# Optimization experiments

Hardware: AMD Instinct MI355X
Metric: run time of the kernel (lower is better)

## Reference

```python
import jax, jax.numpy as jnp
import numpy as np

EPS = 1e-12
ALPHA = 0.5


def mlp(x, W1, b1, W2, b2):
    # 2-layer MLP (dropout inactive in eval mode) + row-wise l2 norm * 10
    h = jax.nn.relu(x @ W1 + b1)
    y = h @ W2 + b2
    n = jnp.maximum(jnp.linalg.norm(y, axis=-1, keepdims=True), EPS)
    return y / n * 10.0


def setup_inputs() -> dict:
    key = jax.random.key(0)
    ks = jax.random.split(key, 12)
    T, N, F = 3, 100000, 128
    M, E = 4, 65536
    B, H, O = 65536, 128, 64
    X = jax.random.normal(ks[0], (T, N, F), dtype=jnp.float32)
    s_features = jax.random.normal(ks[1], (B, F), dtype=jnp.float32)
    features_map = jax.random.randint(ks[2], (T, N), 0, N)
    s_idxs = jax.random.randint(ks[3], (M, T, E), 0, B)
    t_idxs = jax.random.randint(ks[4], (M, T, E), 0, N)
    weightss = jax.random.uniform(ks[5], (M, T, E), dtype=jnp.float32)
    W1 = jax.random.normal(ks[6], (F, H), dtype=jnp.float32) / np.sqrt(F)
    b1 = jnp.zeros((H,), dtype=jnp.float32)
    W2 = jax.random.normal(ks[7], (H, O), dtype=jnp.float32) / np.sqrt(H)
    b2 = jnp.zeros((O,), dtype=jnp.float32)
    metapath_weights = jnp.ones((M,), dtype=jnp.float32)
    ntype_weights = jnp.ones((T,), dtype=jnp.float32)
    return {"X": X, "s_features": s_features, "features_map": features_map,
            "s_idxs": s_idxs, "t_idxs": t_idxs, "weightss": weightss,
            "batch_size": B, "W1": W1, "b1": b1, "W2": W2, "b2": b2,
            "metapath_weights": metapath_weights, "ntype_weights": ntype_weights}


def reference(X, s_features, features_map, s_idxs, t_idxs, weightss,
              batch_size, W1, b1, W2, b2, metapath_weights, ntype_weights):
    M, T, E = s_idxs.shape
    O = W2.shape[1]
    nm = jax.nn.softmax(metapath_weights)  # [M]
    nt = jax.nn.softmax(ntype_weights)     # [T]
    t_arr = jnp.arange(T)[None, :, None]   # [1,T,1]
    map_idx = features_map[t_arr, t_idxs]  # [M,T,E]
    feats = X[t_arr, map_idx]              # [M,T,E,F] gather
    y = mlp(feats, W1, b1, W2, b2)         # [M,T,E,O]
    # fold metapath & type weights into per-edge weights (scatter is linear)
    ew = weightss * nt[None, :, None] * nm[:, None, None]  # [M,T,E]
    contrib = (y * ew[..., None]).reshape(-1, O)
    seg = s_idxs.reshape(-1)
    out = jax.ops.segment_sum(contrib, seg, num_segments=batch_size)  # [B,O]
    out = (1.0 - ALPHA) * out + ALPHA * mlp(s_features, W1, b1, W2, b2)
    return jax.nn.log_softmax(out, axis=1)
```

## Files before the change

### kernel.cpp

```cpp
#include <hip/hip_runtime.h>

#define Fdim 128
#define Hdim 128
#define Odim 64
#define RT 64
#define ECAP 64
#define NMLP 448
#define NSCAT 64
#define EPSV 1e-12f
#define ALPHAV 0.5f

typedef _Float16 h8_t __attribute__((ext_vector_type(8)));
typedef _Float16 h4_t __attribute__((ext_vector_type(4)));
typedef float f32x4 __attribute__((ext_vector_type(4)));

#define W2T_OFF 0
#define X_OFF   16384
#define H_OFF   32768
#define LDS_BYTES 49152
#define WIMG_BYTES 49152

extern "C" __global__ __launch_bounds__(512, 4)
void fused_mlp_scatter(const float* __restrict__ X, const float* __restrict__ S,
                       const char* __restrict__ wimg, const float* __restrict__ b1,
                       const float* __restrict__ b2,
                       _Float16* __restrict__ Yh, float* __restrict__ out,
                       int TN, int rows_total, int ngroups,
                       const int* __restrict__ s_idxs, const int* __restrict__ t_idxs,
                       const float* __restrict__ wss, const int* __restrict__ fmap,
                       const float* __restrict__ mw, const float* __restrict__ tw,
                       int* __restrict__ cnt, int2* __restrict__ edat,
                       int Nn, int Tt, int Mm, int Eslab)
{
    const int tid = threadIdx.x;

    if (blockIdx.x >= NMLP) {
        if (edat == nullptr) return;
        const int sb = blockIdx.x - NMLP;
        float mmax = -1e30f, tmax = -1e30f, msum = 0.f, tsum = 0.f;
        for (int i = 0; i < Mm; ++i) mmax = fmaxf(mmax, mw[i]);
        for (int i = 0; i < Mm; ++i) msum += expf(mw[i] - mmax);
        for (int i = 0; i < Tt; ++i) tmax = fmaxf(tmax, tw[i]);
        for (int i = 0; i < Tt; ++i) tsum += expf(tw[i] - tmax);
        const float inv = (1.0f - ALPHAV) / (msum * tsum);

        const int MT = Mm * Tt;
        for (int slab = 0; slab < MT; ++slab) {
            const int t  = slab % Tt;
            const int tN = t * Nn;
            const float scale = expf(mw[slab / Tt] - mmax) * expf(tw[t] - tmax) * inv;
            for (int i = sb * 512 + tid; i < Eslab; i += NSCAT * 512) {
                int e    = slab * Eslab + i;
                int si   = s_idxs[e];
                int yrow = tN + fmap[tN + t_idxs[e]];
                float w  = wss[e] * scale;
                int pos  = atomicAdd(cnt + si, 1);
                if (pos < ECAP)
                    edat[(size_t)si * ECAP + pos] = make_int2(yrow, __float_as_int(w));
            }
        }
        return;
    }

    extern __shared__ char smem[];
    const int wave = tid >> 6;
    const int lane = tid & 63;
    const int c = lane & 15;
    const int g = lane >> 4;

    #pragma unroll
    for (int i = 0; i < 2; ++i) {
        int idx = tid + i * 512;
        float4 v = *(const float4*)(wimg + 32768 + idx * 16);
        *(float4*)(smem + W2T_OFF + idx * 16) = v;
    }

    h8_t w1f[4];
    {
        int r0 = wave * 16 + c;
        #pragma unroll
        for (int kt = 0; kt < 4; ++kt)
            w1f[kt] = *(const h8_t*)(wimg + (((r0 << 8) + (kt << 6) + (g << 4)) ^ ((c & 7) << 4)));
    }

    const int hbase = wave * 16 + 4 * g;
    float b1v[4];
    #pragma unroll
    for (int j = 0; j < 4; ++j) b1v[j] = b1[hbase + j];
    float bb[4];
    #pragma unroll
    for (int ct = 0; ct < 4; ++ct) bb[ct] = b2[ct * 16 + c];

    float4 pf[4];
    int grp = blockIdx.x;
    #pragma unroll
    for (int it = 0; it < 4; ++it) {
        int idx = tid + it * 512;
        int r = idx >> 5, c4 = idx & 31;
        int rowg = grp * RT + r;
        float4 v = make_float4(0.f, 0.f, 0.f, 0.f);
        if (rowg < TN)               v = *(const float4*)(X + (size_t)rowg * Fdim + c4 * 4);
        else if (rowg < rows_total)  v = *(const float4*)(S + (size_t)(rowg - TN) * Fdim + c4 * 4);
        pf[it] = v;
    }
    #pragma unroll
    for (int it = 0; it < 4; ++it) {
        int idx = tid + it * 512;
        int r = idx >> 5, c4 = idx & 31;
        h4_t hv;
        hv[0] = (_Float16)pf[it].x; hv[1] = (_Float16)pf[it].y;
        hv[2] = (_Float16)pf[it].z; hv[3] = (_Float16)pf[it].w;
        *(h4_t*)(smem + X_OFF + ((r * 256 + c4 * 8) ^ ((r & 7) << 4))) = hv;
    }
    __syncthreads();

    for (; grp < ngroups; grp += NMLP) {
        const int gnext = grp + NMLP;

        #pragma unroll
        for (int it = 0; it < 4; ++it) {
            int idx = tid + it * 512;
            int r = idx >> 5, c4 = idx & 31;
            int rowg = gnext * RT + r;
            float4 v = make_float4(0.f, 0.f, 0.f, 0.f);
            if (rowg < TN)               v = *(const float4*)(X + (size_t)rowg * Fdim + c4 * 4);
            else if (rowg < rows_total)  v = *(const float4*)(S + (size_t)(rowg - TN) * Fdim + c4 * 4);
            pf[it] = v;
        }

        f32x4 acc[4];
        #pragma unroll
        for (int r = 0; r < 4; ++r) acc[r] = (f32x4){0.f, 0.f, 0.f, 0.f};

        #pragma unroll
        for (int kt = 0; kt < 4; ++kt) {
            #pragma unroll
            for (int rt = 0; rt < 4; ++rt) {
                int xr = rt * 16 + c;
                h8_t bf = *(const h8_t*)(smem + X_OFF + ((xr * 256 + kt * 64 + g * 16) ^ ((c & 7) << 4)));
                acc[rt] = __builtin_amdgcn_mfma_f32_16x16x32_f16(w1f[kt], bf, acc[rt], 0, 0, 0);
            }
        }

        #pragma unroll
        for (int rt = 0; rt < 4; ++rt) {
            int xr = rt * 16 + c;
            h4_t hv;
            #pragma unroll
            for (int j = 0; j < 4; ++j) {
                float hval = acc[rt][j] + b1v[j];
                hval = fmaxf(hval, 0.f);
                hv[j] = (_Float16)hval;
            }
            *(h4_t*)(smem + H_OFF + ((xr * 256 + hbase * 2) ^ ((xr & 7) << 4))) = hv;
        }
        __syncthreads();

        if (wave < 4) {
            f32x4 acc2[4];
            #pragma unroll
            for (int ct = 0; ct < 4; ++ct) acc2[ct] = (f32x4){0.f, 0.f, 0.f, 0.f};

            #pragma unroll
            for (int kt = 0; kt < 4; ++kt) {
                int xr = wave * 16 + c;
                h8_t a = *(const h8_t*)(smem + H_OFF + ((xr * 256 + kt * 64 + g * 16) ^ ((xr & 7) << 4)));
                #pragma unroll
                for (int ct = 0; ct < 4; ++ct) {
                    int wr = ct * 16 + c;
                    h8_t bf = *(const h8_t*)(smem + W2T_OFF + ((wr * 256 + kt * 64 + g * 16) ^ ((c & 7) << 4)));
                    acc2[ct] = __builtin_amdgcn_mfma_f32_16x16x32_f16(a, bf, acc2[ct], 0, 0, 0);
                }
            }

            float y[4][4];
            float ssq[4] = {0.f, 0.f, 0.f, 0.f};
            #pragma unroll
            for (int ct = 0; ct < 4; ++ct) {
                #pragma unroll
                for (int j = 0; j < 4; ++j) {
                    float v = acc2[ct][j] + bb[ct];
                    y[ct][j] = v;
                    ssq[j] += v * v;
                }
            }
            #pragma unroll
            for (int j = 0; j < 4; ++j) {
                float s = ssq[j];
                s += __shfl_xor(s, 1);
                s += __shfl_xor(s, 2);
                s += __shfl_xor(s, 4);
                s += __shfl_xor(s, 8);
                float n  = fmaxf(sqrtf(s), EPSV);
                float sc = 10.0f / n;
                int rowg = grp * RT + wave * 16 + 4 * g + j;
                if (rowg < TN) {
                    _Float16* dst = Yh + (size_t)rowg * Odim;
                    #pragma unroll
                    for (int ct = 0; ct < 4; ++ct)
                        dst[ct * 16 + c] = (_Float16)(y[ct][j] * sc);
                } else if (rowg < rows_total) {
                    float* dst = out + (size_t)(rowg - TN) * Odim;
                    #pragma unroll
                    for (int ct = 0; ct < 4; ++ct)
                        dst[ct * 16 + c] = ALPHAV * y[ct][j] * sc;
                }
            }
        }

        #pragma unroll
        for (int it = 0; it < 4; ++it) {
            int idx = tid + it * 512;
            int r = idx >> 5, c4 = idx & 31;
            h4_t hv;
            hv[0] = (_Float16)pf[it].x; hv[1] = (_Float16)pf[it].y;
            hv[2] = (_Float16)pf[it].z; hv[3] = (_Float16)pf[it].w;
            *(h4_t*)(smem + X_OFF + ((r * 256 + c4 * 8) ^ ((r & 7) << 4))) = hv;
        }
        __syncthreads();
    }
}

extern "C" __global__ __launch_bounds__(256)
void prep_all(const float* __restrict__ W1, const float* __restrict__ W2,
              char* __restrict__ wimg, int* __restrict__ cnt, int B)
{
    if (blockIdx.x < 96) {
        int idx = blockIdx.x * 256 + threadIdx.x;
        if (idx < 16384) {
            int h = idx >> 7, f = idx & 127;
            float v = W1[(size_t)f * Hdim + h];
            int byte = (h * 256 + f * 2) ^ ((h & 7) << 4);
            *(_Float16*)(wimg + byte) = (_Float16)v;
        } else if (idx < 24576) {
            int i2 = idx - 16384;
            int o = i2 >> 7, k = i2 & 127;
            float v = W2[(size_t)k * Odim + o];
            int byte = 32768 + ((o * 256 + k * 2) ^ ((o & 7) << 4));
            *(_Float16*)(wimg + byte) = (_Float16)v;
        }
    } else {
        int i = (blockIdx.x - 96) * 256 + threadIdx.x;
        if (i < B) cnt[i] = 0;
    }
}

extern "C" __global__ __launch_bounds__(256)
void row_gather(const int2* __restrict__ edgedat, const int* __restrict__ cnt,
                const _Float16* __restrict__ Yh, float* __restrict__ out, int B)
{
    const int lane = threadIdx.x & 63;
    const int grp8 = lane >> 3;
    const int sub  = lane & 7;
    int b = blockIdx.x * 4 + (threadIdx.x >> 6);
    if (b >= B) return;
    int n = cnt[b];
    if (n > ECAP) n = ECAP;
    const int2* ebase = edgedat + (size_t)b * ECAP;

    float acc[8];
    #pragma unroll
    for (int j = 0; j < 8; ++j) acc[j] = 0.f;

    for (int e = grp8; e < n; e += 8) {
        int2 ed = ebase[e];
        float w = __int_as_float(ed.y);
        h8_t y8 = *(const h8_t*)(Yh + (size_t)ed.x * Odim + sub * 8);
        #pragma unroll
        for (int j = 0; j < 8; ++j) acc[j] += w * (float)y8[j];
    }
    #pragma unroll
    for (int d = 8; d < 64; d <<= 1) {
        #pragma unroll
        for (int j = 0; j < 8; ++j) acc[j] += __shfl_xor(acc[j], d);
    }
    const float* orow = out + (size_t)b * Odim + sub * 8;
    float v[8];
    #pragma unroll
    for (int j = 0; j < 8; ++j) v[j] = orow[j] + acc[j];

    float mx = v[0];
    #pragma unroll
    for (int j = 1; j < 8; ++j) mx = fmaxf(mx, v[j]);
    #pragma unroll
    for (int d = 1; d < 8; d <<= 1) mx = fmaxf(mx, __shfl_xor(mx, d));
    float sm = 0.f;
    #pragma unroll
    for (int j = 0; j < 8; ++j) sm += expf(v[j] - mx);
    #pragma unroll
    for (int d = 1; d < 8; d <<= 1) sm += __shfl_xor(sm, d);
    float lg = mx + logf(sm);

    if (grp8 == 0) {
        float* dst = out + (size_t)b * Odim + sub * 8;
        #pragma unroll
        for (int j = 0; j < 8; ++j) dst[j] = v[j] - lg;
    }
}


extern "C" __global__ __launch_bounds__(256)
void edge_scatter(const int* __restrict__ s_idxs, const int* __restrict__ t_idxs,
                  const float* __restrict__ weightss, const int* __restrict__ fmap,
                  const _Float16* __restrict__ Yh, const float* __restrict__ mw,
                  const float* __restrict__ tw,
                  float* __restrict__ out, int Nn, int Tt, int Mm, int Eslab)
{
    const int lane = threadIdx.x & 63;
    const int slab = blockIdx.y;
    const int t    = slab % Tt;
    const int tN   = t * Nn;
    float mmax = -1e30f, tmax = -1e30f, msum = 0.f, tsum = 0.f;
    for (int i = 0; i < Mm; ++i) mmax = fmaxf(mmax, mw[i]);
    for (int i = 0; i < Mm; ++i) msum += expf(mw[i] - mmax);
    for (int i = 0; i < Tt; ++i) tmax = fmaxf(tmax, tw[i]);
    for (int i = 0; i < Tt; ++i) tsum += expf(tw[i] - tmax);
    const float scale = (1.0f - ALPHAV) * expf(mw[slab / Tt] - mmax) * expf(tw[t] - tmax)
                        / (msum * tsum);

    const int wid  = blockIdx.x * (blockDim.x >> 6) + (threadIdx.x >> 6);
    const int off  = wid * 64;
    if (off >= Eslab) return;

    const int ebase = slab * Eslab + off;
    int   e_ok = (off + lane) < Eslab;
    int   eidx = ebase + (e_ok ? lane : 0);
    int   si   = s_idxs[eidx];
    int   ti   = t_idxs[eidx];
    float w    = e_ok ? (weightss[eidx] * scale) : 0.0f;
    int   yrow = tN + fmap[tN + ti];

    #pragma unroll 8
    for (int i = 0; i < 64; ++i) {
        int   nd = __builtin_amdgcn_readlane(yrow, i);
        int   s  = __builtin_amdgcn_readlane(si, i);
        float ws = __uint_as_float(__builtin_amdgcn_readlane(__float_as_uint(w), i));
        float yv = (float)Yh[(size_t)nd * Odim + lane];
        atomicAdd(out + (size_t)s * Odim + lane, yv * ws);
    }
}

extern "C" __global__ __launch_bounds__(256)
void log_softmax_rows(float* __restrict__ out, int Brows)
{
    int lane = threadIdx.x & 63;
    int r = blockIdx.x * 4 + (threadIdx.x >> 6);
    if (r >= Brows) return;
    float* row = out + (size_t)r * Odim;
    float v = row[lane];
    float mx = v;
    for (int off = 32; off > 0; off >>= 1) mx = fmaxf(mx, __shfl_xor(mx, off));
    float ex = expf(v - mx);
    float s = ex;
    for (int off = 32; off > 0; off >>= 1) s += __shfl_xor(s, off);
    row[lane] = v - mx - logf(s);
}

extern "C" void kernel_launch(void* const* d_in, const int* in_sizes, int n_in,
                              void* d_out, int out_size, void* d_ws, size_t ws_size,
                              hipStream_t stream)
{
    const float* X   = (const float*)d_in[0];
    const float* S   = (const float*)d_in[1];
    const int*   fmap= (const int*)d_in[2];
    const int*   sidx= (const int*)d_in[3];
    const int*   tidx= (const int*)d_in[4];
    const float* wss = (const float*)d_in[5];
    const float* W1  = (const float*)d_in[7];
    const float* b1  = (const float*)d_in[8];
    const float* W2  = (const float*)d_in[9];
    const float* b2  = (const float*)d_in[10];
    const float* mw  = (const float*)d_in[11];
    const float* tw  = (const float*)d_in[12];
    float* out = (float*)d_out;

    const int M = in_sizes[11];
    const int T = in_sizes[12];
    const int H = in_sizes[8];
    const int Fv = in_sizes[7] / H;
    const int N = in_sizes[2] / T;
    const int nedges = in_sizes[3];
    const int E = nedges / (M * T);
    const int B = in_sizes[1] / Fv;
    const int TN = T * N;
    const int rows_total = TN + B;
    const int ngroups = (rows_total + RT - 1) / RT;

    char* wp = (char*)d_ws;
    size_t used = 0;
    auto alloc = [&](size_t bytes) -> char* {
        char* p = wp + used;
        used = (used + bytes + 255) & ~(size_t)255;
        return p;
    };
    _Float16* Yh   = (_Float16*)alloc((size_t)TN * Odim * sizeof(_Float16));
    char*     wimg = (char*)    alloc((size_t)WIMG_BYTES);
    int*      cntp = (int*)     alloc((size_t)B * sizeof(int));
    int2*     edat = (int2*)    alloc((size_t)B * ECAP * sizeof(int2));
    bool bucket_ok = used <= ws_size;

    hipFuncSetAttribute((const void*)fused_mlp_scatter,
                        hipFuncAttributeMaxDynamicSharedMemorySize, LDS_BYTES);

    const int zb = (B + 255) / 256;
    prep_all<<<96 + zb, 256, 0, stream>>>(W1, W2, wimg, cntp, B);

    if (bucket_ok) {
        fused_mlp_scatter<<<NMLP + NSCAT, 512, LDS_BYTES, stream>>>(
            X, S, wimg, b1, b2, Yh, out, TN, rows_total, ngroups,
            sidx, tidx, wss, fmap, mw, tw, cntp, edat, N, T, M, E);
        row_gather<<<(B + 3) / 4, 256, 0, stream>>>(edat, cntp, Yh, out, B);
    } else {
        fused_mlp_scatter<<<NMLP + NSCAT, 512, LDS_BYTES, stream>>>(
            X, S, wimg, b1, b2, Yh, out, TN, rows_total, ngroups,
            sidx, tidx, wss, fmap, mw, tw, cntp, nullptr, N, T, M, E);
        int waves_per_slab = (E + 63) / 64;
        dim3 sg((waves_per_slab + 3) / 4, M * T);
        edge_scatter<<<sg, 256, 0, stream>>>(sidx, tidx, wss, fmap, Yh, mw, tw, out,
                                             N, T, M, E);
        log_softmax_rows<<<(B + 3) / 4, 256, 0, stream>>>(out, B);
    }
}
```

Baseline: 147.6 us.

## Split edge bucketing into its own kernel and double-buffer MLP LDS tiles

Moves edge bucketing out of the fused MLP kernel into a separate fully parallel scatter_edges kernel (one thread per edge, one grid row per slab) that runs before the MLP. The MLP kernel now uses double-buffered X and H tiles in LDS, so the next tile is written before the barrier and one __syncthreads per iteration is dropped. Its grid becomes 512 blocks with a gridDim stride. LDS grows from 48KB to 80KB, which may cut occupancy, and the bucketing no longer overlaps with MLP work.

```diff
diff --git a/kernel.cpp b/kernel.cpp
--- a/kernel.cpp
+++ b/kernel.cpp
@@ -5,8 +5,6 @@
 #define Odim 64
 #define RT 64
 #define ECAP 64
-#define NMLP 448
-#define NSCAT 64
 #define EPSV 1e-12f
 #define ALPHAV 0.5f
 
@@ -15,54 +13,20 @@
 typedef float f32x4 __attribute__((ext_vector_type(4)));
 
 #define W2T_OFF 0
-#define X_OFF   16384
-#define H_OFF   32768
-#define LDS_BYTES 49152
+#define X0_OFF  16384
+#define H0_OFF  49152
+#define LDS_BYTES 81920
 #define WIMG_BYTES 49152
 
 extern "C" __global__ __launch_bounds__(512, 4)
-void fused_mlp_scatter(const float* __restrict__ X, const float* __restrict__ S,
-                       const char* __restrict__ wimg, const float* __restrict__ b1,
-                       const float* __restrict__ b2,
-                       _Float16* __restrict__ Yh, float* __restrict__ out,
-                       int TN, int rows_total, int ngroups,
-                       const int* __restrict__ s_idxs, const int* __restrict__ t_idxs,
-                       const float* __restrict__ wss, const int* __restrict__ fmap,
-                       const float* __restrict__ mw, const float* __restrict__ tw,
-                       int* __restrict__ cnt, int2* __restrict__ edat,
-                       int Nn, int Tt, int Mm, int Eslab)
-{
-    const int tid = threadIdx.x;
-
-    if (blockIdx.x >= NMLP) {
-        if (edat == nullptr) return;
-        const int sb = blockIdx.x - NMLP;
-        float mmax = -1e30f, tmax = -1e30f, msum = 0.f, tsum = 0.f;
-        for (int i = 0; i < Mm; ++i) mmax = fmaxf(mmax, mw[i]);
-        for (int i = 0; i < Mm; ++i) msum += expf(mw[i] - mmax);
-        for (int i = 0; i < Tt; ++i) tmax = fmaxf(tmax, tw[i]);
-        for (int i = 0; i < Tt; ++i) tsum += expf(tw[i] - tmax);
-        const float inv = (1.0f - ALPHAV) / (msum * tsum);
-
-        const int MT = Mm * Tt;
-        for (int slab = 0; slab < MT; ++slab) {
-            const int t  = slab % Tt;
-            const int tN = t * Nn;
-            const float scale = expf(mw[slab / Tt] - mmax) * expf(tw[t] - tmax) * inv;
-            for (int i = sb * 512 + tid; i < Eslab; i += NSCAT * 512) {
-                int e    = slab * Eslab + i;
-                int si   = s_idxs[e];
-                int yrow = tN + fmap[tN + t_idxs[e]];
-                float w  = wss[e] * scale;
-                int pos  = atomicAdd(cnt + si, 1);
-                if (pos < ECAP)
-                    edat[(size_t)si * ECAP + pos] = make_int2(yrow, __float_as_int(w));
-            }
-        }
-        return;
-    }
-
+void mlp_all(const float* __restrict__ X, const float* __restrict__ S,
+             const char* __restrict__ wimg, const float* __restrict__ b1,
+             const float* __restrict__ b2,
+             _Float16* __restrict__ Yh, float* __restrict__ out,
+             int TN, int rows_total, int ngroups)
+{
     extern __shared__ char smem[];
+    const int tid  = threadIdx.x;
     const int wave = tid >> 6;
     const int lane = tid & 63;
     const int c = lane & 15;
@@ -110,12 +74,16 @@
         h4_t hv;
         hv[0] = (_Float16)pf[it].x; hv[1] = (_Float16)pf[it].y;
         hv[2] = (_Float16)pf[it].z; hv[3] = (_Float16)pf[it].w;
-        *(h4_t*)(smem + X_OFF + ((r * 256 + c4 * 8) ^ ((r & 7) << 4))) = hv;
+        *(h4_t*)(smem + X0_OFF + ((r * 256 + c4 * 8) ^ ((r & 7) << 4))) = hv;
     }
     __syncthreads();
 
-    for (; grp < ngroups; grp += NMLP) {
-        const int gnext = grp + NMLP;
+    int cur = 0;
+    for (; grp < ngroups; grp += gridDim.x, cur ^= 1) {
+        const int gnext = grp + gridDim.x;
+        const int xb = X0_OFF + cur * 16384;
+        const int hb = H0_OFF + cur * 16384;
+        const int xn = X0_OFF + (cur ^ 1) * 16384;
 
         #pragma unroll
         for (int it = 0; it < 4; ++it) {
@@ -137,7 +105,7 @@
             #pragma unroll
             for (int rt = 0; rt < 4; ++rt) {
                 int xr = rt * 16 + c;
-                h8_t bf = *(const h8_t*)(smem + X_OFF + ((xr * 256 + kt * 64 + g * 16) ^ ((c & 7) << 4)));
+                h8_t bf = *(const h8_t*)(smem + xb + ((xr * 256 + kt * 64 + g * 16) ^ ((c & 7) << 4)));
                 acc[rt] = __builtin_amdgcn_mfma_f32_16x16x32_f16(w1f[kt], bf, acc[rt], 0, 0, 0);
             }
         }
@@ -152,8 +120,19 @@
                 hval = fmaxf(hval, 0.f);
                 hv[j] = (_Float16)hval;
             }
-            *(h4_t*)(smem + H_OFF + ((xr * 256 + hbase * 2) ^ ((xr & 7) << 4))) = hv;
-        }
+            *(h4_t*)(smem + hb + ((xr * 256 + hbase * 2) ^ ((xr & 7) << 4))) = hv;
+        }
+
+        #pragma unroll
+        for (int it = 0; it < 4; ++it) {
+            int idx = tid + it * 512;
+            int r = idx >> 5, c4 = idx & 31;
+            h4_t hv;
+            hv[0] = (_Float16)pf[it].x; hv[1] = (_Float16)pf[it].y;
+            hv[2] = (_Float16)pf[it].z; hv[3] = (_Float16)pf[it].w;
+            *(h4_t*)(smem + xn + ((r * 256 + c4 * 8) ^ ((r & 7) << 4))) = hv;
+        }
+
         __syncthreads();
 
         if (wave < 4) {
@@ -164,7 +143,7 @@
             #pragma unroll
             for (int kt = 0; kt < 4; ++kt) {
                 int xr = wave * 16 + c;
-                h8_t a = *(const h8_t*)(smem + H_OFF + ((xr * 256 + kt * 64 + g * 16) ^ ((xr & 7) << 4)));
+                h8_t a = *(const h8_t*)(smem + hb + ((xr * 256 + kt * 64 + g * 16) ^ ((xr & 7) << 4)));
                 #pragma unroll
                 for (int ct = 0; ct < 4; ++ct) {
                     int wr = ct * 16 + c;
@@ -207,17 +186,6 @@
                 }
             }
         }
-
-        #pragma unroll
-        for (int it = 0; it < 4; ++it) {
-            int idx = tid + it * 512;
-            int r = idx >> 5, c4 = idx & 31;
-            h4_t hv;
-            hv[0] = (_Float16)pf[it].x; hv[1] = (_Float16)pf[it].y;
-            hv[2] = (_Float16)pf[it].z; hv[3] = (_Float16)pf[it].w;
-            *(h4_t*)(smem + X_OFF + ((r * 256 + c4 * 8) ^ ((r & 7) << 4))) = hv;
-        }
-        __syncthreads();
     }
 }
 
@@ -246,6 +214,35 @@
 }
 
 extern "C" __global__ __launch_bounds__(256)
+void scatter_edges(const int* __restrict__ s_idxs, const int* __restrict__ t_idxs,
+                   const float* __restrict__ wss, const int* __restrict__ fmap,
+                   const float* __restrict__ mw, const float* __restrict__ tw,
+                   int* __restrict__ cnt, int2* __restrict__ edat,
+                   int Nn, int Tt, int Mm, int Eslab)
+{
+    const int slab = blockIdx.y;
+    const int t    = slab % Tt;
+    const int tN   = t * Nn;
+    float mmax = -1e30f, tmax = -1e30f, msum = 0.f, tsum = 0.f;
+    for (int i = 0; i < Mm; ++i) mmax = fmaxf(mmax, mw[i]);
+    for (int i = 0; i < Mm; ++i) msum += expf(mw[i] - mmax);
+    for (int i = 0; i < Tt; ++i) tmax = fmaxf(tmax, tw[i]);
+    for (int i = 0; i < Tt; ++i) tsum += expf(tw[i] - tmax);
+    const float scale = (1.0f - ALPHAV) * expf(mw[slab / Tt] - mmax) * expf(tw[t] - tmax)
+                        / (msum * tsum);
+
+    int i = blockIdx.x * 256 + threadIdx.x;
+    if (i >= Eslab) return;
+    int e = slab * Eslab + i;
+    int si   = s_idxs[e];
+    int yrow = tN + fmap[tN + t_idxs[e]];
+    float w  = wss[e] * scale;
+    int pos = atomicAdd(cnt + si, 1);
+    if (pos < ECAP)
+        edat[(size_t)si * ECAP + pos] = make_int2(yrow, __float_as_int(w));
+}
+
+extern "C" __global__ __launch_bounds__(256)
 void row_gather(const int2* __restrict__ edgedat, const int* __restrict__ cnt,
                 const _Float16* __restrict__ Yh, float* __restrict__ out, int B)
 {
@@ -399,21 +396,22 @@
     int2*     edat = (int2*)    alloc((size_t)B * ECAP * sizeof(int2));
     bool bucket_ok = used <= ws_size;
 
-    hipFuncSetAttribute((const void*)fused_mlp_scatter,
+    hipFuncSetAttribute((const void*)mlp_all,
                         hipFuncAttributeMaxDynamicSharedMemorySize, LDS_BYTES);
 
     const int zb = (B + 255) / 256;
     prep_all<<<96 + zb, 256, 0, stream>>>(W1, W2, wimg, cntp, B);
 
     if (bucket_ok) {
-        fused_mlp_scatter<<<NMLP + NSCAT, 512, LDS_BYTES, stream>>>(
-            X, S, wimg, b1, b2, Yh, out, TN, rows_total, ngroups,
-            sidx, tidx, wss, fmap, mw, tw, cntp, edat, N, T, M, E);
+        dim3 sg((E + 255) / 256, M * T);
+        scatter_edges<<<sg, 256, 0, stream>>>(sidx, tidx, wss, fmap, mw, tw,
+                                              cntp, edat, N, T, M, E);
+        mlp_all<<<512, 512, LDS_BYTES, stream>>>(X, S, wimg, b1, b2, Yh, out,
+                                                 TN, rows_total, ngroups);
         row_gather<<<(B + 3) / 4, 256, 0, stream>>>(edat, cntp, Yh, out, B);
     } else {
-        fused_mlp_scatter<<<NMLP + NSCAT, 512, LDS_BYTES, stream>>>(
-            X, S, wimg, b1, b2, Yh, out, TN, rows_total, ngroups,
-            sidx, tidx, wss, fmap, mw, tw, cntp, nullptr, N, T, M, E);
+        mlp_all<<<512, 512, LDS_BYTES, stream>>>(X, S, wimg, b1, b2, Yh, out,
+                                                 TN, rows_total, ngroups);
         int waves_per_slab = (E + 63) / 64;
         dim3 sg((waves_per_slab + 3) / 4, M * T);
         edge_scatter<<<sg, 256, 0, stream>>>(sidx, tidx, wss, fmap, Yh, mw, tw, out,
```

New measurement: 146.1 us, median of 2. About the same (-1.0%).
